# Optimization experiments

Hardware: AMD Instinct MI355X
Metric: run time of the kernel (lower is better)

## Reference

```python
import jax, jax.numpy as jnp
import numpy as np

HID, HEADS, FFN = 2048, 16, 8192
HEAD_DIM = HID // HEADS
B, S = 2, 2048
EPS = 1e-5


def setup_inputs() -> dict:
    key = jax.random.key(0)
    ks = jax.random.split(key, 12)
    s = 0.02
    x = jax.random.normal(ks[0], (B, S, HID), dtype=jnp.float32)
    # additive causal mask: 0 on/below diagonal, -inf-like above
    neg = jnp.float32(-1e9)
    causal = jnp.where(jnp.tril(jnp.ones((S, S), dtype=bool)), 0.0, neg)
    mask = causal[None, None, :, :].astype(jnp.float32)
    return {
        "x": x,
        "mask": mask,
        "ln1_w": jnp.ones((HID,), jnp.float32),
        "ln1_b": jnp.zeros((HID,), jnp.float32),
        "q_w": jax.random.normal(ks[1], (HID, HID), jnp.float32) * s,
        "k_w": jax.random.normal(ks[2], (HID, HID), jnp.float32) * s,
        "v_w": jax.random.normal(ks[3], (HID, HID), jnp.float32) * s,
        "o_w": jax.random.normal(ks[4], (HID, HID), jnp.float32) * s,
        "ln2_w": jnp.ones((HID,), jnp.float32),
        "ln2_b": jnp.zeros((HID,), jnp.float32),
        "w1_w": jax.random.normal(ks[5], (FFN, HID), jnp.float32) * s,
        "w1_b": jnp.zeros((FFN,), jnp.float32),
        "wg_w": jax.random.normal(ks[6], (FFN, HID), jnp.float32) * s,
        "w2_w": jax.random.normal(ks[7], (HID, FFN), jnp.float32) * s,
        "w2_b": jnp.zeros((HID,), jnp.float32),
    }


def _layernorm(x, w, b):
    mu = jnp.mean(x, axis=-1, keepdims=True)
    var = jnp.mean(jnp.square(x - mu), axis=-1, keepdims=True)
    return (x - mu) * jax.lax.rsqrt(var + EPS) * w + b


def reference(x, mask, ln1_w, ln1_b, q_w, k_w, v_w, o_w,
              ln2_w, ln2_b, w1_w, w1_b, wg_w, w2_w, w2_b):
    b, s, _ = x.shape
    # --- attention sublayer ---
    h = _layernorm(x, ln1_w, ln1_b)
    def split_heads(y):  # [b,s,hid] -> [b,H,s,d]
        return y.reshape(b, s, HEADS, HEAD_DIM).transpose(0, 2, 1, 3)
    q = split_heads(h @ q_w.T)
    k = split_heads(h @ k_w.T)
    v = split_heads(h @ v_w.T)
    scale = jnp.sqrt(jnp.float32(HEAD_DIM))
    scores = jnp.einsum('bhqd,bhkd->bhqk', q, k) / scale + mask
    weights = jax.nn.softmax(scores, axis=-1)
    attn = jnp.einsum('bhqk,bhkd->bhqd', weights, v)
    attn = attn.transpose(0, 2, 1, 3).reshape(b, s, HID)
    x = x + attn @ o_w.T
    # --- SwiGLU FFN sublayer ---
    h2 = _layernorm(x, ln2_w, ln2_b)
    ff = jax.nn.silu(h2 @ w1_w.T + w1_b) * (h2 @ wg_w.T)
    x = x + ff @ w2_w.T + w2_b
    return x
```

## Files before the change

### kernel.cpp

```cpp
#include <hip/hip_runtime.h>
#include <cstdint>
#include <cstddef>

#define HIDN 2048
#define NROWS 4096
#define FFND 8192
#define SEQ 2048
#define QKVN 6144

typedef __attribute__((ext_vector_type(8))) __bf16 bf16x8;
typedef __attribute__((ext_vector_type(4))) float f32x4;

__device__ __forceinline__ unsigned short f2b(float f) {
    union { float f; unsigned u; } v; v.f = f;
    unsigned r = v.u + 0x7fffu + ((v.u >> 16) & 1u);
    return (unsigned short)(r >> 16);
}
__device__ __forceinline__ float b2f(unsigned short h) {
    union { unsigned u; float f; } v; v.u = ((unsigned)h) << 16; return v.f;
}
__device__ __forceinline__ void gload16(const void* g, void* lds) {
    __builtin_amdgcn_global_load_lds(
        (const __attribute__((address_space(1))) void*)g,
        (__attribute__((address_space(3))) void*)lds, 16, 0, 0);
}

__global__ __launch_bounds__(256) void convall_kernel(
    const float* __restrict__ s0, const float* __restrict__ s1,
    const float* __restrict__ s2, const float* __restrict__ s3,
    const float* __restrict__ s4, const float* __restrict__ s5,
    const float* __restrict__ s6, unsigned short* __restrict__ dst) {
    const int M1 = 1 << 20;
    int i = blockIdx.x * 256 + threadIdx.x;
    const float* src; int rel;
    if      (i <  1 * M1) { src = s0; rel = i;          }
    else if (i <  2 * M1) { src = s1; rel = i - 1 * M1; }
    else if (i <  3 * M1) { src = s2; rel = i - 2 * M1; }
    else if (i <  4 * M1) { src = s3; rel = i - 3 * M1; }
    else if (i <  8 * M1) { src = s4; rel = i - 4 * M1; }
    else if (i < 12 * M1) { src = s5; rel = i - 8 * M1; }
    else                  { src = s6; rel = i - 12 * M1; }
    float4 v = ((const float4*)src)[rel];
    ushort4 o;
    o.x = f2b(v.x); o.y = f2b(v.y); o.z = f2b(v.z); o.w = f2b(v.w);
    ((ushort4*)dst)[i] = o;
}

__global__ __launch_bounds__(256) void ln_kernel(const float* __restrict__ x,
                                                 const float* __restrict__ w,
                                                 const float* __restrict__ b,
                                                 unsigned short* __restrict__ out) {
    int row = blockIdx.x, tid = threadIdx.x;
    const float4* xr = (const float4*)(x + (size_t)row * HIDN);
    float4 a0 = xr[tid], a1 = xr[tid + 256];
    float s  = a0.x + a0.y + a0.z + a0.w + a1.x + a1.y + a1.z + a1.w;
    float s2 = a0.x*a0.x + a0.y*a0.y + a0.z*a0.z + a0.w*a0.w
             + a1.x*a1.x + a1.y*a1.y + a1.z*a1.z + a1.w*a1.w;
#pragma unroll
    for (int i = 1; i < 64; i <<= 1) { s += __shfl_xor(s, i); s2 += __shfl_xor(s2, i); }
    __shared__ float red[8];
    if ((tid & 63) == 0) { red[tid >> 6] = s; red[4 + (tid >> 6)] = s2; }
    __syncthreads();
    s  = red[0] + red[1] + red[2] + red[3];
    s2 = red[4] + red[5] + red[6] + red[7];
    float mu  = s * (1.0f / HIDN);
    float var = s2 * (1.0f / HIDN) - mu * mu;
    float rstd = rsqrtf(var + 1e-5f);
    const float4* wv = (const float4*)w;
    const float4* bv = (const float4*)b;
    float4 w0 = wv[tid], w1 = wv[tid + 256], b0 = bv[tid], b1 = bv[tid + 256];
    ushort4 o0, o1;
    o0.x = f2b((a0.x - mu) * rstd * w0.x + b0.x);
    o0.y = f2b((a0.y - mu) * rstd * w0.y + b0.y);
    o0.z = f2b((a0.z - mu) * rstd * w0.z + b0.z);
    o0.w = f2b((a0.w - mu) * rstd * w0.w + b0.w);
    o1.x = f2b((a1.x - mu) * rstd * w1.x + b1.x);
    o1.y = f2b((a1.y - mu) * rstd * w1.y + b1.y);
    o1.z = f2b((a1.z - mu) * rstd * w1.z + b1.z);
    o1.w = f2b((a1.w - mu) * rstd * w1.w + b1.w);
    ushort4* orow = (ushort4*)(out + (size_t)row * HIDN);
    orow[tid] = o0; orow[tid + 256] = o1;
}

template <int EPI>
__global__ __launch_bounds__(256)
void gemm_bt(const unsigned short* __restrict__ A, const unsigned short* __restrict__ Bw,
             int M, int N, int K, int tiles_n, float scale,
             const float* __restrict__ bias, const float* __restrict__ resf,
             const unsigned short* __restrict__ aux,
             float* __restrict__ outf, unsigned short* __restrict__ outb) {
    __shared__ unsigned short Asm[2][128 * 32];
    __shared__ unsigned short Bsm[2][128 * 32];
    int tid = threadIdx.x;
    int wave = tid >> 6, lane = tid & 63;
    int lrow = lane & 15, quad = lane >> 4;
    int nchunk = tiles_n >> 3;
    int xcd = blockIdx.x & 7;
    int pxi = blockIdx.x >> 3;
    int bn = xcd * nchunk + pxi % nchunk;
    int bm = pxi / nchunk;
    int wm = (wave >> 1) * 64, wn = (wave & 1) * 64;

    f32x4 acc[4][4];
#pragma unroll
    for (int i = 0; i < 4; i++)
#pragma unroll
        for (int j = 0; j < 4; j++) acc[i][j] = f32x4{0.f, 0.f, 0.f, 0.f};

    int srow = wave * 32 + (lane >> 2);
    int scol = (lane & 3) * 8;
    const unsigned short* Ag = A + (size_t)(bm * 128 + srow) * K + scol;
    const unsigned short* Bg = Bw + (size_t)(bn * 128 + srow) * K + scol;

    for (int k0 = 0; k0 < K; k0 += 64) {
#pragma unroll
        for (int s = 0; s < 2; s++) {
            gload16(Ag + k0 + s * 32, &Asm[s][(wave * 2 + 0) * 512]);
            gload16(Ag + k0 + s * 32 + (size_t)16 * K, &Asm[s][(wave * 2 + 1) * 512]);
            gload16(Bg + k0 + s * 32, &Bsm[s][(wave * 2 + 0) * 512]);
            gload16(Bg + k0 + s * 32 + (size_t)16 * K, &Bsm[s][(wave * 2 + 1) * 512]);
        }
        __syncthreads();
#pragma unroll
        for (int s = 0; s < 2; s++) {
            bf16x8 af[4], bfb[4];
#pragma unroll
            for (int mi = 0; mi < 4; mi++)
                af[mi] = *(const bf16x8*)&Asm[s][(wm + mi * 16 + lrow) * 32 + quad * 8];
#pragma unroll
            for (int ni = 0; ni < 4; ni++)
                bfb[ni] = *(const bf16x8*)&Bsm[s][(wn + ni * 16 + lrow) * 32 + quad * 8];
#pragma unroll
            for (int mi = 0; mi < 4; mi++)
#pragma unroll
                for (int ni = 0; ni < 4; ni++)
                    acc[mi][ni] = __builtin_amdgcn_mfma_f32_16x16x32_bf16(af[mi], bfb[ni], acc[mi][ni], 0, 0, 0);
        }
        __syncthreads();
    }

    int row0 = bm * 128 + wm, col0 = bn * 128 + wn;
#pragma unroll
    for (int mi = 0; mi < 4; mi++) {
#pragma unroll
        for (int ni = 0; ni < 4; ni++) {
            int c = col0 + ni * 16 + lrow;
#pragma unroll
            for (int r = 0; r < 4; r++) {
                int rr = row0 + mi * 16 + quad * 4 + r;
                size_t idx = (size_t)rr * N + c;
                float vv = acc[mi][ni][r];
                if constexpr (EPI == 0) {
                    outb[idx] = f2b(vv * scale);
                } else if constexpr (EPI == 1) {
                    outf[idx] = vv + resf[idx];
                } else if constexpr (EPI == 2) {
                    outb[idx] = f2b(vv + bias[c]);
                } else if constexpr (EPI == 3) {
                    float av = b2f(aux[idx]);
                    float sl = av / (1.f + __expf(-av));
                    outb[idx] = f2b(sl * vv);
                } else if constexpr (EPI == 4) {
                    outf[idx] = vv + bias[c] + resf[idx];
                } else if constexpr (EPI == 5) {
                    outb[idx] = f2b(vv * (c < HIDN ? scale : 1.0f));
                }
            }
        }
    }
}

__global__ __launch_bounds__(256)
void attn_kernel(const unsigned short* __restrict__ qkv, unsigned short* __restrict__ o) {
    int bh = blockIdx.x;
    int qt = 31 - blockIdx.y;
    int b = bh >> 4, h = bh & 15;
    int tid = threadIdx.x, wave = tid >> 6, lane = tid & 63;
    int lrow = lane & 15, quad = lane >> 4;
    int q0 = qt * 64;
    size_t base = ((size_t)b * SEQ) * QKVN + h * 128;
    const unsigned short* qp0 = qkv + base;
    const unsigned short* kp0 = qkv + base + HIDN;
    const unsigned short* vp0 = qkv + base + 2 * HIDN;
    size_t obase = ((size_t)b * SEQ) * HIDN + h * 128;

    __shared__ unsigned short Ksm[64 * 136];
    __shared__ unsigned short VTsm[128 * 72];
    __shared__ unsigned short Psm[4 * 16 * 72];

    bf16x8 qf[4];
    {
        const unsigned short* qp = qp0 + (size_t)(q0 + wave * 16 + lrow) * QKVN + quad * 8;
#pragma unroll
        for (int kc = 0; kc < 4; kc++) qf[kc] = *(const bf16x8*)(qp + kc * 32);
    }

    f32x4 oacc[8];
#pragma unroll
    for (int i = 0; i < 8; i++) oacc[i] = f32x4{0.f, 0.f, 0.f, 0.f};
    float m_run[4], l_run[4];
    int rowg[4];
#pragma unroll
    for (int r = 0; r < 4; r++) {
        m_run[r] = -1e30f; l_run[r] = 0.f;
        rowg[r] = q0 + wave * 16 + quad * 4 + r;
    }

    for (int kt = 0; kt <= qt; ++kt) {
        {
            int r = tid >> 2, cc = (tid & 3) * 32;
            const uint4* src = (const uint4*)(kp0 + (size_t)(kt * 64 + r) * QKVN + cc);
            uint4* dst = (uint4*)&Ksm[r * 136 + cc];
            dst[0] = src[0]; dst[1] = src[1]; dst[2] = src[2]; dst[3] = src[3];
        }
        {
            int kv = (tid >> 3) * 2, d0 = (tid & 7) * 16;
            const unsigned short* vp = vp0 + (size_t)(kt * 64 + kv) * QKVN + d0;
            unsigned short va[16], vb[16];
            *(uint4*)&va[0] = ((const uint4*)vp)[0];
            *(uint4*)&va[8] = ((const uint4*)vp)[1];
            *(uint4*)&vb[0] = ((const uint4*)(vp + QKVN))[0];
            *(uint4*)&vb[8] = ((const uint4*)(vp + QKVN))[1];
#pragma unroll
            for (int i = 0; i < 16; i++) {
                unsigned pair = (unsigned)va[i] | ((unsigned)vb[i] << 16);
                *(unsigned*)&VTsm[(d0 + i) * 72 + kv] = pair;
            }
        }
        __syncthreads();

        f32x4 sacc[4];
#pragma unroll
        for (int ns = 0; ns < 4; ns++) sacc[ns] = f32x4{0.f, 0.f, 0.f, 0.f};
#pragma unroll
        for (int ns = 0; ns < 4; ns++) {
            const unsigned short* kb = &Ksm[(ns * 16 + lrow) * 136 + quad * 8];
#pragma unroll
            for (int kc = 0; kc < 4; kc++) {
                bf16x8 kf = *(const bf16x8*)(kb + kc * 32);
                sacc[ns] = __builtin_amdgcn_mfma_f32_16x16x32_bf16(qf[kc], kf, sacc[ns], 0, 0, 0);
            }
        }
#pragma unroll
        for (int ns = 0; ns < 4; ns++) {
            int colg = kt * 64 + ns * 16 + lrow;
#pragma unroll
            for (int r = 0; r < 4; r++)
                if (colg > rowg[r]) sacc[ns][r] = -1e30f;
        }
        float mnew[4], alpha[4], rsum[4];
#pragma unroll
        for (int r = 0; r < 4; r++) {
            float mv = fmaxf(fmaxf(sacc[0][r], sacc[1][r]), fmaxf(sacc[2][r], sacc[3][r]));
#pragma unroll
            for (int off = 1; off < 16; off <<= 1) mv = fmaxf(mv, __shfl_xor(mv, off));
            mnew[r] = fmaxf(m_run[r], mv);
            alpha[r] = __expf(m_run[r] - mnew[r]);
            rsum[r] = 0.f;
        }
#pragma unroll
        for (int ns = 0; ns < 4; ns++)
#pragma unroll
            for (int r = 0; r < 4; r++) {
                float p = __expf(sacc[ns][r] - mnew[r]);
                sacc[ns][r] = p;
                rsum[r] += p;
            }
#pragma unroll
        for (int r = 0; r < 4; r++) {
#pragma unroll
            for (int off = 1; off < 16; off <<= 1) rsum[r] += __shfl_xor(rsum[r], off);
            l_run[r] = l_run[r] * alpha[r] + rsum[r];
            m_run[r] = mnew[r];
        }
#pragma unroll
        for (int nc = 0; nc < 8; nc++)
#pragma unroll
            for (int r = 0; r < 4; r++) oacc[nc][r] *= alpha[r];

        unsigned short* pw = &Psm[wave * 16 * 72];
#pragma unroll
        for (int ns = 0; ns < 4; ns++)
#pragma unroll
            for (int r = 0; r < 4; r++)
                pw[(quad * 4 + r) * 72 + ns * 16 + lrow] = f2b(sacc[ns][r]);
        asm volatile("s_waitcnt lgkmcnt(0)" ::: "memory");
        bf16x8 pf[2];
#pragma unroll
        for (int kc = 0; kc < 2; kc++)
            pf[kc] = *(const bf16x8*)&pw[lrow * 72 + kc * 32 + quad * 8];
#pragma unroll
        for (int nc = 0; nc < 8; nc++) {
#pragma unroll
            for (int kc = 0; kc < 2; kc++) {
                bf16x8 vf = *(const bf16x8*)&VTsm[(nc * 16 + lrow) * 72 + kc * 32 + quad * 8];
                oacc[nc] = __builtin_amdgcn_mfma_f32_16x16x32_bf16(pf[kc], vf, oacc[nc], 0, 0, 0);
            }
        }
        __syncthreads();
    }

    float inv[4];
#pragma unroll
    for (int r = 0; r < 4; r++) inv[r] = 1.f / l_run[r];
#pragma unroll
    for (int nc = 0; nc < 8; nc++) {
#pragma unroll
        for (int r = 0; r < 4; r++) {
            int srow = q0 + wave * 16 + quad * 4 + r;
            o[obase + (size_t)srow * HIDN + nc * 16 + lrow] = f2b(oacc[nc][r] * inv[r]);
        }
    }
}

extern "C" void kernel_launch(void* const* d_in, const int* in_sizes, int n_in,
                              void* d_out, int out_size, void* d_ws, size_t ws_size,
                              hipStream_t stream) {
    const float* x    = (const float*)d_in[0];
    const float* ln1w = (const float*)d_in[2];
    const float* ln1b = (const float*)d_in[3];
    const float* qw   = (const float*)d_in[4];
    const float* kw   = (const float*)d_in[5];
    const float* vw   = (const float*)d_in[6];
    const float* ow   = (const float*)d_in[7];
    const float* ln2w = (const float*)d_in[8];
    const float* ln2b = (const float*)d_in[9];
    const float* w1w  = (const float*)d_in[10];
    const float* w1bias = (const float*)d_in[11];
    const float* wgw  = (const float*)d_in[12];
    const float* w2w  = (const float*)d_in[13];
    const float* w2bias = (const float*)d_in[14];
    float* out = (float*)d_out;

    char* ws = (char*)d_ws;
    const size_t MB = 1ull << 20;
    unsigned short* wall  = (unsigned short*)(ws + 0 * MB);
    unsigned short* qkvwb = (unsigned short*)(ws + 0 * MB);
    unsigned short* owb  = (unsigned short*)(ws + 24 * MB);
    unsigned short* w1wb = (unsigned short*)(ws + 32 * MB);
    unsigned short* wgwb = (unsigned short*)(ws + 64 * MB);
    unsigned short* w2wb = (unsigned short*)(ws + 96 * MB);
    unsigned short* a1   = (unsigned short*)(ws + 128 * MB);
    unsigned short* hbuf = (unsigned short*)(ws + 128 * MB);
    unsigned short* qkvb = (unsigned short*)(ws + 144 * MB);
    unsigned short* attnb= (unsigned short*)(ws + 192 * MB);
    unsigned short* h2   = (unsigned short*)(ws + 208 * MB);
    float*          x1   = out;

    convall_kernel<<<65536, 256, 0, stream>>>(qw, kw, vw, ow, w1w, wgw, w2w, wall);

    ln_kernel<<<NROWS, 256, 0, stream>>>(x, ln1w, ln1b, hbuf);

    const float qscale = 0.08838834764831845f;
    gemm_bt<5><<<dim3(32 * 48), 256, 0, stream>>>(hbuf, qkvwb, NROWS, QKVN, HIDN, 48, qscale,
                                                  nullptr, nullptr, nullptr, nullptr, qkvb);
    attn_kernel<<<dim3(32, 32), 256, 0, stream>>>(qkvb, attnb);
    gemm_bt<1><<<dim3(32 * 16), 256, 0, stream>>>(attnb, owb, NROWS, HIDN, HIDN, 16, 1.0f,
                                                  nullptr, x, nullptr, x1, nullptr);
    ln_kernel<<<NROWS, 256, 0, stream>>>(x1, ln2w, ln2b, h2);
    gemm_bt<2><<<dim3(32 * 64), 256, 0, stream>>>(h2, w1wb, NROWS, FFND, HIDN, 64, 1.0f,
                                                  w1bias, nullptr, nullptr, nullptr, a1);
    gemm_bt<3><<<dim3(32 * 64), 256, 0, stream>>>(h2, wgwb, NROWS, FFND, HIDN, 64, 1.0f,
                                                  nullptr, nullptr, a1, nullptr, a1);
    gemm_bt<4><<<dim3(32 * 16), 256, 0, stream>>>(a1, w2wb, NROWS, HIDN, FFND, 16, 1.0f,
                                                  w2bias, x1, nullptr, out, nullptr);
    (void)in_sizes; (void)n_in; (void)out_size; (void)ws_size;
}
```

Before: 1.148 ms.

## Replace GEMM with 256x256-tile, 8-wave kernel using 4-stage LDS prefetch pipeline

Replaces the 128x128 double-buffered GEMM with a 256x256-tile kernel using 512 threads. The K loop now runs over 32-wide slabs through a 4-deep ring of LDS buffers, prefetched three steps ahead with explicit vmcnt waits, raw barriers and s_setprio around the MFMA bursts. The aim is more data reuse per tile and global-load latency hidden behind compute. In exchange it uses more LDS and accumulator registers per block and launches fewer blocks, which may underfill the GPU for the smaller N=2048 GEMMs (128 blocks).

```diff
diff --git a/kernel.cpp b/kernel.cpp
--- a/kernel.cpp
+++ b/kernel.cpp
@@ -83,73 +83,108 @@
 }
 
 template <int EPI>
-__global__ __launch_bounds__(256)
-void gemm_bt(const unsigned short* __restrict__ A, const unsigned short* __restrict__ Bw,
+__global__ __launch_bounds__(512)
+void gemm256(const unsigned short* __restrict__ A, const unsigned short* __restrict__ Bw,
              int M, int N, int K, int tiles_n, float scale,
              const float* __restrict__ bias, const float* __restrict__ resf,
              const unsigned short* __restrict__ aux,
              float* __restrict__ outf, unsigned short* __restrict__ outb) {
-    __shared__ unsigned short Asm[2][128 * 32];
-    __shared__ unsigned short Bsm[2][128 * 32];
+    __shared__ unsigned short lds[4][2][8192];
     int tid = threadIdx.x;
     int wave = tid >> 6, lane = tid & 63;
     int lrow = lane & 15, quad = lane >> 4;
+    int wm = wave >> 2, wn = wave & 3;
     int nchunk = tiles_n >> 3;
     int xcd = blockIdx.x & 7;
     int pxi = blockIdx.x >> 3;
     int bn = xcd * nchunk + pxi % nchunk;
     int bm = pxi / nchunk;
-    int wm = (wave >> 1) * 64, wn = (wave & 1) * 64;
-
-    f32x4 acc[4][4];
-#pragma unroll
-    for (int i = 0; i < 4; i++)
+
+    f32x4 acc[8][4];
+#pragma unroll
+    for (int i = 0; i < 8; i++)
 #pragma unroll
         for (int j = 0; j < 4; j++) acc[i][j] = f32x4{0.f, 0.f, 0.f, 0.f};
 
-    int srow = wave * 32 + (lane >> 2);
+    int srow = wave * 16 + (lane >> 2);
     int scol = (lane & 3) * 8;
-    const unsigned short* Ag = A + (size_t)(bm * 128 + srow) * K + scol;
-    const unsigned short* Bg = Bw + (size_t)(bn * 128 + srow) * K + scol;
-
-    for (int k0 = 0; k0 < K; k0 += 64) {
-#pragma unroll
-        for (int s = 0; s < 2; s++) {
-            gload16(Ag + k0 + s * 32, &Asm[s][(wave * 2 + 0) * 512]);
-            gload16(Ag + k0 + s * 32 + (size_t)16 * K, &Asm[s][(wave * 2 + 1) * 512]);
-            gload16(Bg + k0 + s * 32, &Bsm[s][(wave * 2 + 0) * 512]);
-            gload16(Bg + k0 + s * 32 + (size_t)16 * K, &Bsm[s][(wave * 2 + 1) * 512]);
-        }
-        __syncthreads();
-#pragma unroll
-        for (int s = 0; s < 2; s++) {
-            bf16x8 af[4], bfb[4];
-#pragma unroll
-            for (int mi = 0; mi < 4; mi++)
-                af[mi] = *(const bf16x8*)&Asm[s][(wm + mi * 16 + lrow) * 32 + quad * 8];
+    const unsigned short* Ag = A + (size_t)(bm * 256 + srow) * K + scol;
+    const unsigned short* Bg = Bw + (size_t)(bn * 256 + srow) * K + scol;
+    const int NT = K >> 5;
+
+    auto stage = [&](int slab, int part) {
+        const unsigned short* g = part ? Bg : Ag;
+        unsigned short* lb = &lds[slab & 3][part][wave * 512];
+        size_t koff = (size_t)slab << 5;
+        gload16(g + koff, lb);
+        gload16(g + koff + (size_t)128 * K, lb + 4096);
+    };
+
+    stage(0, 0); stage(0, 1);
+    stage(1, 0); stage(1, 1);
+    stage(2, 0); stage(2, 1);
+    asm volatile("s_waitcnt vmcnt(8)" ::: "memory");
+    __builtin_amdgcn_s_barrier();
+    asm volatile("" ::: "memory");
+
+#pragma unroll 1
+    for (int t = 0; t < NT; ++t) {
+        const unsigned short* Abuf = &lds[t & 3][0][0];
+        const unsigned short* Bbuf = &lds[t & 3][1][0];
+        bf16x8 bfr[4], afr[4];
+#pragma unroll
+        for (int ni = 0; ni < 4; ni++)
+            bfr[ni] = *(const bf16x8*)&Bbuf[(wn * 64 + ni * 16 + lrow) * 32 + quad * 8];
+#pragma unroll
+        for (int mi = 0; mi < 4; mi++)
+            afr[mi] = *(const bf16x8*)&Abuf[(wm * 128 + mi * 16 + lrow) * 32 + quad * 8];
+        if (t + 3 < NT) stage(t + 3, 0);
+        __builtin_amdgcn_s_barrier();
+        asm volatile("s_waitcnt lgkmcnt(0)" ::: "memory");
+        __builtin_amdgcn_s_setprio(1);
+#pragma unroll
+        for (int mi = 0; mi < 4; mi++)
 #pragma unroll
             for (int ni = 0; ni < 4; ni++)
-                bfb[ni] = *(const bf16x8*)&Bsm[s][(wn + ni * 16 + lrow) * 32 + quad * 8];
-#pragma unroll
-            for (int mi = 0; mi < 4; mi++)
-#pragma unroll
-                for (int ni = 0; ni < 4; ni++)
-                    acc[mi][ni] = __builtin_amdgcn_mfma_f32_16x16x32_bf16(af[mi], bfb[ni], acc[mi][ni], 0, 0, 0);
-        }
-        __syncthreads();
-    }
-
-    int row0 = bm * 128 + wm, col0 = bn * 128 + wn;
-#pragma unroll
-    for (int mi = 0; mi < 4; mi++) {
+                acc[mi][ni] = __builtin_amdgcn_mfma_f32_16x16x32_bf16(afr[mi], bfr[ni], acc[mi][ni], 0, 0, 0);
+        __builtin_amdgcn_s_setprio(0);
+        __builtin_amdgcn_s_barrier();
+        asm volatile("" ::: "memory");
+#pragma unroll
+        for (int mi = 0; mi < 4; mi++)
+            afr[mi] = *(const bf16x8*)&Abuf[(wm * 128 + 64 + mi * 16 + lrow) * 32 + quad * 8];
+        if (t + 3 < NT) {
+            stage(t + 3, 1);
+            asm volatile("s_waitcnt vmcnt(8)" ::: "memory");
+        } else if (t + 2 < NT) {
+            asm volatile("s_waitcnt vmcnt(4)" ::: "memory");
+        } else if (t + 1 < NT) {
+            asm volatile("s_waitcnt vmcnt(0)" ::: "memory");
+        }
+        __builtin_amdgcn_s_barrier();
+        asm volatile("s_waitcnt lgkmcnt(0)" ::: "memory");
+        __builtin_amdgcn_s_setprio(1);
+#pragma unroll
+        for (int mi = 0; mi < 4; mi++)
+#pragma unroll
+            for (int ni = 0; ni < 4; ni++)
+                acc[4 + mi][ni] = __builtin_amdgcn_mfma_f32_16x16x32_bf16(afr[mi], bfr[ni], acc[4 + mi][ni], 0, 0, 0);
+        __builtin_amdgcn_s_setprio(0);
+        __builtin_amdgcn_s_barrier();
+        asm volatile("" ::: "memory");
+    }
+
+    int row0 = bm * 256 + wm * 128, col0 = bn * 256 + wn * 64;
+#pragma unroll
+    for (int mi8 = 0; mi8 < 8; mi8++) {
+        int rbase = row0 + (mi8 >> 2) * 64 + (mi8 & 3) * 16 + quad * 4;
 #pragma unroll
         for (int ni = 0; ni < 4; ni++) {
             int c = col0 + ni * 16 + lrow;
 #pragma unroll
             for (int r = 0; r < 4; r++) {
-                int rr = row0 + mi * 16 + quad * 4 + r;
-                size_t idx = (size_t)rr * N + c;
-                float vv = acc[mi][ni][r];
+                size_t idx = (size_t)(rbase + r) * N + c;
+                float vv = acc[mi8][ni][r];
                 if constexpr (EPI == 0) {
                     outb[idx] = f2b(vv * scale);
                 } else if constexpr (EPI == 1) {
@@ -168,6 +203,7 @@
             }
         }
     }
+    (void)M;
 }
 
 __global__ __launch_bounds__(256)
@@ -352,17 +388,17 @@
     ln_kernel<<<NROWS, 256, 0, stream>>>(x, ln1w, ln1b, hbuf);
 
     const float qscale = 0.08838834764831845f;
-    gemm_bt<5><<<dim3(32 * 48), 256, 0, stream>>>(hbuf, qkvwb, NROWS, QKVN, HIDN, 48, qscale,
+    gemm256<5><<<dim3(16 * 24), 512, 0, stream>>>(hbuf, qkvwb, NROWS, QKVN, HIDN, 24, qscale,
                                                   nullptr, nullptr, nullptr, nullptr, qkvb);
     attn_kernel<<<dim3(32, 32), 256, 0, stream>>>(qkvb, attnb);
-    gemm_bt<1><<<dim3(32 * 16), 256, 0, stream>>>(attnb, owb, NROWS, HIDN, HIDN, 16, 1.0f,
-                                                  nullptr, x, nullptr, x1, nullptr);
+    gemm256<1><<<dim3(16 * 8), 512, 0, stream>>>(attnb, owb, NROWS, HIDN, HIDN, 8, 1.0f,
+                                                 nullptr, x, nullptr, x1, nullptr);
     ln_kernel<<<NROWS, 256, 0, stream>>>(x1, ln2w, ln2b, h2);
-    gemm_bt<2><<<dim3(32 * 64), 256, 0, stream>>>(h2, w1wb, NROWS, FFND, HIDN, 64, 1.0f,
+    gemm256<2><<<dim3(16 * 32), 512, 0, stream>>>(h2, w1wb, NROWS, FFND, HIDN, 32, 1.0f,
                                                   w1bias, nullptr, nullptr, nullptr, a1);
-    gemm_bt<3><<<dim3(32 * 64), 256, 0, stream>>>(h2, wgwb, NROWS, FFND, HIDN, 64, 1.0f,
+    gemm256<3><<<dim3(16 * 32), 512, 0, stream>>>(h2, wgwb, NROWS, FFND, HIDN, 32, 1.0f,
                                                   nullptr, nullptr, a1, nullptr, a1);
-    gemm_bt<4><<<dim3(32 * 16), 256, 0, stream>>>(a1, w2wb, NROWS, HIDN, FFND, 16, 1.0f,
-                                                  w2bias, x1, nullptr, out, nullptr);
+    gemm256<4><<<dim3(16 * 8), 512, 0, stream>>>(a1, w2wb, NROWS, HIDN, FFND, 8, 1.0f,
+                                                 w2bias, x1, nullptr, out, nullptr);
     (void)in_sizes; (void)n_in; (void)out_size; (void)ws_size;
 }
```

After: 1.151 ms. About the same (+0.3%).
